# Performance work log

Measured on AMD Instinct MI355X. Metric: run time of the kernel, lower is better.

The kernel has to match this reference:

```python
import jax, jax.numpy as jnp
import numpy as np

N = 20000
E = 320000
IN_FEAT = 256
HID = 256
OUT_FEAT = 128


def setup_inputs() -> dict:
    key = jax.random.key(0)
    ks = jax.random.split(key, 10)
    inp = {
        "x": jax.random.normal(ks[0], (N, IN_FEAT), dtype=jnp.float32),
        "edge_src": jax.random.randint(ks[1], (E,), 0, N, dtype=jnp.int32),
        "edge_dst": jax.random.randint(ks[2], (E,), 0, N, dtype=jnp.int32),
        "edge_w": jax.random.uniform(ks[3], (E,), dtype=jnp.float32),
        # params (Linear weights stored as [out, in], torch convention)
        "W_emb": jax.random.normal(ks[4], (HID, IN_FEAT), dtype=jnp.float32) / np.sqrt(IN_FEAT),
        "W_gc1": jax.random.normal(ks[5], (HID, 2 * HID), dtype=jnp.float32) / np.sqrt(2 * HID),
        "b_gc1": jnp.zeros((HID,), dtype=jnp.float32),
        "W_gc2": jax.random.normal(ks[6], (HID, 2 * HID), dtype=jnp.float32) / np.sqrt(2 * HID),
        "b_gc2": jnp.zeros((HID,), dtype=jnp.float32),
        "W_fc": jax.random.normal(ks[7], (OUT_FEAT, HID), dtype=jnp.float32) / np.sqrt(HID),
    }
    return inp


def reference(x, edge_src, edge_dst, edge_w, W_emb, W_gc1, b_gc1, W_gc2, b_gc2, W_fc):
    n = x.shape[0]

    def adj_mul(h):
        msgs = h[edge_src] * edge_w[:, None]           # [E, hid]
        return jax.ops.segment_sum(msgs, edge_dst, num_segments=n)

    def gconv(h, W, b):
        cat = jnp.concatenate([h, adj_mul(h)], axis=1)  # [N, 2*hid]
        return cat @ W.T + b

    h = x @ W_emb.T                                    # embedding (no bias)
    h = h + jax.nn.relu(gconv(h, W_gc1, b_gc1))        # residual (dropout = eval identity)
    h = h + jax.nn.relu(gconv(h, W_gc2, b_gc2))
    out = h @ W_fc.T                                   # fc_last (no bias)
    out = out / jnp.sqrt(jnp.sum(out * out, axis=1, keepdims=True))
    return out
```

## Files before the change

### kernel.cpp

```cpp
#include <hip/hip_runtime.h>
#include <math.h>

#define N_NODES 20000
#define E_EDGES 320000
#define HID 256
#define OUT_FEAT 128
#define MPAD 20224
#define CAP 64

#define BK 64
#define LSTR 72

typedef __attribute__((ext_vector_type(8))) __bf16 bf16x8;
typedef __attribute__((ext_vector_type(4))) float floatx4;


#define EMB_BLK 632
#define SCAT_BLK 1250
#define CONV_BLK 144

__global__ __launch_bounds__(256) void front_kernel(
    const float* __restrict__ x,
    const float* __restrict__ wembf,
    __bf16* __restrict__ hb0,
    const int* __restrict__ src, const int* __restrict__ dst,
    const float* __restrict__ w, int* __restrict__ counts,
    int2* __restrict__ edges,
    const float* __restrict__ w1f, const float* __restrict__ w2f,
    const float* __restrict__ wfcf,
    __bf16* __restrict__ w1b, __bf16* __restrict__ w2b,
    __bf16* __restrict__ wfcb)
{
    __shared__ __bf16 As[64 * LSTR];
    __shared__ __bf16 Bs[128 * LSTR];
    const int bid = blockIdx.x;
    const int tid = threadIdx.x;

    if (bid < EMB_BLK) {
        const int row0 = (bid >> 1) * 64;
        const int col0 = (bid & 1) * 128;
        const int wv = tid >> 6, l = tid & 63, lr = l & 15, lq = l >> 4;
        const int wm = wv & 1, wn = wv >> 1;

        floatx4 acc[2][4];
#pragma unroll
        for (int i = 0; i < 2; i++)
#pragma unroll
            for (int j = 0; j < 4; j++) acc[i][j] = (floatx4){0.f, 0.f, 0.f, 0.f};

        const int srow = tid >> 3;
        const int skq = (tid & 7) * 8;

        for (int kc = 0; kc < 256; kc += BK) {
#pragma unroll
            for (int r = 0; r < 2; r++) {
                int row = r * 32 + srow;
                int grow = row0 + row;
                float4 v0 = make_float4(0.f, 0.f, 0.f, 0.f), v1 = v0;
                if (grow < N_NODES) {
                    const float* xp = x + (size_t)grow * HID + kc + skq;
                    v0 = *(const float4*)xp;
                    v1 = *(const float4*)(xp + 4);
                }
                bf16x8 o;
                o[0] = (__bf16)v0.x; o[1] = (__bf16)v0.y; o[2] = (__bf16)v0.z; o[3] = (__bf16)v0.w;
                o[4] = (__bf16)v1.x; o[5] = (__bf16)v1.y; o[6] = (__bf16)v1.z; o[7] = (__bf16)v1.w;
                *(bf16x8*)&As[row * LSTR + skq] = o;
            }
#pragma unroll
            for (int r = 0; r < 4; r++) {
                int row = r * 32 + srow;
                const float* wp = wembf + (size_t)(col0 + row) * 256 + kc + skq;
                float4 v0 = *(const float4*)wp;
                float4 v1 = *(const float4*)(wp + 4);
                bf16x8 o;
                o[0] = (__bf16)v0.x; o[1] = (__bf16)v0.y; o[2] = (__bf16)v0.z; o[3] = (__bf16)v0.w;
                o[4] = (__bf16)v1.x; o[5] = (__bf16)v1.y; o[6] = (__bf16)v1.z; o[7] = (__bf16)v1.w;
                *(bf16x8*)&Bs[row * LSTR + skq] = o;
            }
            __syncthreads();
#pragma unroll
            for (int s = 0; s < 2; s++) {
                bf16x8 af[2], bfr[4];
#pragma unroll
                for (int mt = 0; mt < 2; mt++)
                    af[mt] = *(const bf16x8*)&As[(wm * 32 + mt * 16 + lr) * LSTR + s * 32 + lq * 8];
#pragma unroll
                for (int nt = 0; nt < 4; nt++)
                    bfr[nt] = *(const bf16x8*)&Bs[(wn * 64 + nt * 16 + lr) * LSTR + s * 32 + lq * 8];
#pragma unroll
                for (int mt = 0; mt < 2; mt++)
#pragma unroll
                    for (int nt = 0; nt < 4; nt++)
                        acc[mt][nt] = __builtin_amdgcn_mfma_f32_16x16x32_bf16(af[mt], bfr[nt], acc[mt][nt], 0, 0, 0);
            }
            __syncthreads();
        }
#pragma unroll
        for (int nt = 0; nt < 4; nt++) {
            const int col = col0 + wn * 64 + nt * 16 + lr;
#pragma unroll
            for (int mt = 0; mt < 2; mt++) {
                const int row = row0 + wm * 32 + mt * 16 + lq * 4;
#pragma unroll
                for (int r = 0; r < 4; r++)
                    hb0[(size_t)(row + r) * HID + col] = (__bf16)acc[mt][nt][r];
            }
        }
    } else if (bid < EMB_BLK + SCAT_BLK) {
        int e = (bid - EMB_BLK) * 256 + tid;
        int d = dst[e];
        int p = atomicAdd(&counts[d], 1);
        edges[(size_t)d * CAP + p] = make_int2(src[e], __float_as_int(w[e]));
    } else {
        const size_t gi = ((size_t)(bid - EMB_BLK - SCAT_BLK) * 256 + tid) * 8;
        const size_t s1 = 131072, s2 = 262144;
        const float* srcp; __bf16* dstp; size_t off;
        if (gi < s1)      { srcp = w1f; dstp = w1b; off = gi; }
        else if (gi < s2) { srcp = w2f; dstp = w2b; off = gi - s1; }
        else              { srcp = wfcf; dstp = wfcb; off = gi - s2; }
        float4 v0 = *(const float4*)(srcp + off);
        float4 v1 = *(const float4*)(srcp + off + 4);
        bf16x8 o;
        o[0] = (__bf16)v0.x; o[1] = (__bf16)v0.y; o[2] = (__bf16)v0.z; o[3] = (__bf16)v0.w;
        o[4] = (__bf16)v1.x; o[5] = (__bf16)v1.y; o[6] = (__bf16)v1.z; o[7] = (__bf16)v1.w;
        *(bf16x8*)(dstp + off) = o;
    }
}


__global__ __launch_bounds__(256) void aggregate_kernel(
    const __bf16* __restrict__ h, const int* __restrict__ counts,
    const int2* __restrict__ edges, __bf16* __restrict__ agg) {
    const int w = threadIdx.x >> 6, lane = threadIdx.x & 63;
    const int half = lane >> 5, lh = lane & 31;
    const int d = blockIdx.x * 8 + w * 2 + half;
    const size_t base = (size_t)d * CAP;
    const int cnt = counts[d];
    const int iters = (cnt + 15) >> 4;
    float acc[8];
#pragma unroll
    for (int q = 0; q < 8; q++) acc[q] = 0.f;

    for (int it = 0; it < iters; ++it) {
        const int jb = it * 16;
        const int2* ep = edges + base + jb;
        int4 eh[8];
#pragma unroll
        for (int u = 0; u < 8; u++) eh[u] = *(const int4*)(ep + u * 2);
        int sidx[16]; float wv[16];
#pragma unroll
        for (int u = 0; u < 8; u++) {
            const bool m0 = (jb + u * 2)     < cnt;
            const bool m1 = (jb + u * 2 + 1) < cnt;
            sidx[u * 2]     = m0 ? eh[u].x : 0;
            wv[u * 2]       = m0 ? __int_as_float(eh[u].y) : 0.f;
            sidx[u * 2 + 1] = m1 ? eh[u].z : 0;
            wv[u * 2 + 1]   = m1 ? __int_as_float(eh[u].w) : 0.f;
        }
        bf16x8 hv[16];
#pragma unroll
        for (int u = 0; u < 16; u++)
            hv[u] = *(const bf16x8*)(h + (size_t)sidx[u] * HID + lh * 8);
#pragma unroll
        for (int u = 0; u < 16; u++) {
#pragma unroll
            for (int q = 0; q < 8; q++)
                acc[q] = fmaf(wv[u], (float)hv[u][q], acc[q]);
        }
    }
    bf16x8 o;
#pragma unroll
    for (int q = 0; q < 8; q++) o[q] = (__bf16)acc[q];
    *(bf16x8*)(agg + (size_t)d * HID + lh * 8) = o;
}


__global__ __launch_bounds__(256) void gconv1_kernel(
    const __bf16* __restrict__ hp,
    const __bf16* __restrict__ ag,
    const __bf16* __restrict__ W,
    const float* __restrict__ bias,
    __bf16* __restrict__ hn)
{
    __shared__ __bf16 As[64 * LSTR];
    __shared__ __bf16 Bs[128 * LSTR];
    const int tid = threadIdx.x;
    const int row0 = blockIdx.y * 64;
    const int col0 = blockIdx.x * 128;
    const int wv = tid >> 6, l = tid & 63, lr = l & 15, lq = l >> 4;
    const int wm = wv & 1, wn = wv >> 1;

    floatx4 acc[2][4];
#pragma unroll
    for (int i = 0; i < 2; i++)
#pragma unroll
        for (int j = 0; j < 4; j++) acc[i][j] = (floatx4){0.f, 0.f, 0.f, 0.f};

    const int srow = tid >> 3;
    const int skq = (tid & 7) * 8;

    for (int kc = 0; kc < 512; kc += BK) {
        const __bf16* Asrc = (kc >= 256) ? ag : hp;
        const int ks = kc & 255;
#pragma unroll
        for (int r = 0; r < 2; r++) {
            int row = r * 32 + srow;
            *(bf16x8*)&As[row * LSTR + skq] =
                *(const bf16x8*)(Asrc + (size_t)(row0 + row) * HID + ks + skq);
        }
#pragma unroll
        for (int r = 0; r < 4; r++) {
            int row = r * 32 + srow;
            *(bf16x8*)&Bs[row * LSTR + skq] =
                *(const bf16x8*)(W + (size_t)(col0 + row) * 512 + kc + skq);
        }
        __syncthreads();
#pragma unroll
        for (int s = 0; s < 2; s++) {
            bf16x8 af[2], bfr[4];
#pragma unroll
            for (int mt = 0; mt < 2; mt++)
                af[mt] = *(const bf16x8*)&As[(wm * 32 + mt * 16 + lr) * LSTR + s * 32 + lq * 8];
#pragma unroll
            for (int nt = 0; nt < 4; nt++)
                bfr[nt] = *(const bf16x8*)&Bs[(wn * 64 + nt * 16 + lr) * LSTR + s * 32 + lq * 8];
#pragma unroll
            for (int mt = 0; mt < 2; mt++)
#pragma unroll
                for (int nt = 0; nt < 4; nt++)
                    acc[mt][nt] = __builtin_amdgcn_mfma_f32_16x16x32_bf16(af[mt], bfr[nt], acc[mt][nt], 0, 0, 0);
        }
        __syncthreads();
    }

#pragma unroll
    for (int nt = 0; nt < 4; nt++) {
        const int col = col0 + wn * 64 + nt * 16 + lr;
        const float b = bias[col];
#pragma unroll
        for (int mt = 0; mt < 2; mt++) {
            const int row = row0 + wm * 32 + mt * 16 + lq * 4;
#pragma unroll
            for (int r = 0; r < 4; r++) {
                float res = (float)hp[(size_t)(row + r) * HID + col];
                float v = res + fmaxf(acc[mt][nt][r] + b, 0.f);
                hn[(size_t)(row + r) * HID + col] = (__bf16)v;
            }
        }
    }
}


#define TSTR 264

__global__ __launch_bounds__(512) void gconv_fc_kernel(
    const __bf16* __restrict__ hp,
    const __bf16* __restrict__ ag,
    const __bf16* __restrict__ W,
    const float* __restrict__ bias,
    const __bf16* __restrict__ Wfc,
    float* __restrict__ outp)
{
    __shared__ __bf16 smem[64 * LSTR + 256 * LSTR];
    __bf16* As = smem;
    __bf16* Bs = smem + 64 * LSTR;
    const int tid = threadIdx.x;
    const int row0 = blockIdx.x * 64;
    const int wv = tid >> 6, l = tid & 63, lr = l & 15, lq = l >> 4;
    const int wm = wv & 1, wn4 = wv >> 1;

    floatx4 acc[2][4];
#pragma unroll
    for (int i = 0; i < 2; i++)
#pragma unroll
        for (int j = 0; j < 4; j++) acc[i][j] = (floatx4){0.f, 0.f, 0.f, 0.f};

    const int srow = tid >> 3;
    const int skq = (tid & 7) * 8;

    for (int kc = 0; kc < 512; kc += BK) {
        const __bf16* Asrc = (kc >= 256) ? ag : hp;
        const int ks = kc & 255;
        *(bf16x8*)&As[srow * LSTR + skq] =
            *(const bf16x8*)(Asrc + (size_t)(row0 + srow) * HID + ks + skq);
#pragma unroll
        for (int r = 0; r < 4; r++) {
            int row = r * 64 + srow;
            *(bf16x8*)&Bs[row * LSTR + skq] =
                *(const bf16x8*)(W + (size_t)row * 512 + kc + skq);
        }
        __syncthreads();
#pragma unroll
        for (int s = 0; s < 2; s++) {
            bf16x8 af[2], bfr[4];
#pragma unroll
            for (int mt = 0; mt < 2; mt++)
                af[mt] = *(const bf16x8*)&As[(wm * 32 + mt * 16 + lr) * LSTR + s * 32 + lq * 8];
#pragma unroll
            for (int nt = 0; nt < 4; nt++)
                bfr[nt] = *(const bf16x8*)&Bs[(wn4 * 64 + nt * 16 + lr) * LSTR + s * 32 + lq * 8];
#pragma unroll
            for (int mt = 0; mt < 2; mt++)
#pragma unroll
                for (int nt = 0; nt < 4; nt++)
                    acc[mt][nt] = __builtin_amdgcn_mfma_f32_16x16x32_bf16(af[mt], bfr[nt], acc[mt][nt], 0, 0, 0);
        }
        __syncthreads();
    }

    __bf16 (*tile)[TSTR] = (__bf16(*)[TSTR])smem;
#pragma unroll
    for (int nt = 0; nt < 4; nt++) {
        const int col = wn4 * 64 + nt * 16 + lr;
        const float b = bias[col];
#pragma unroll
        for (int mt = 0; mt < 2; mt++) {
            const int lrow = wm * 32 + mt * 16 + lq * 4;
#pragma unroll
            for (int r = 0; r < 4; r++) {
                float res = (float)hp[(size_t)(row0 + lrow + r) * HID + col];
                float v = res + fmaxf(acc[mt][nt][r] + b, 0.f);
                tile[lrow + r][col] = (__bf16)v;
            }
        }
    }
    __syncthreads();

    if (wv < 4) {
        floatx4 facc[8];
#pragma unroll
        for (int j = 0; j < 8; j++) facc[j] = (floatx4){0.f, 0.f, 0.f, 0.f};
#pragma unroll
        for (int kt = 0; kt < 256; kt += 32) {
            bf16x8 a = *(const bf16x8*)&tile[wv * 16 + lr][kt + lq * 8];
            bf16x8 bf8[8];
#pragma unroll
            for (int nt = 0; nt < 8; nt++)
                bf8[nt] = *(const bf16x8*)(Wfc + (size_t)(nt * 16 + lr) * 256 + kt + lq * 8);
#pragma unroll
            for (int nt = 0; nt < 8; nt++)
                facc[nt] = __builtin_amdgcn_mfma_f32_16x16x32_bf16(a, bf8[nt], facc[nt], 0, 0, 0);
        }
        float s[4];
#pragma unroll
        for (int r = 0; r < 4; r++) {
            float t = 0.f;
#pragma unroll
            for (int nt = 0; nt < 8; nt++) t = fmaf(facc[nt][r], facc[nt][r], t);
            s[r] = t;
        }
#pragma unroll
        for (int mask = 1; mask <= 8; mask <<= 1) {
#pragma unroll
            for (int r = 0; r < 4; r++) s[r] += __shfl_xor(s[r], mask);
        }
        float inv[4];
#pragma unroll
        for (int r = 0; r < 4; r++) inv[r] = rsqrtf(s[r]);
#pragma unroll
        for (int r = 0; r < 4; r++) {
            int row = row0 + wv * 16 + lq * 4 + r;
            if (row >= N_NODES) continue;
#pragma unroll
            for (int nt = 0; nt < 8; nt++)
                outp[(size_t)row * OUT_FEAT + nt * 16 + lr] = facc[nt][r] * inv[r];
        }
    }
}


extern "C" void kernel_launch(void* const* d_in, const int* in_sizes, int n_in,
                              void* d_out, int out_size, void* d_ws, size_t ws_size,
                              hipStream_t stream) {
    const float* x        = (const float*)d_in[0];
    const int*   edge_src = (const int*)d_in[1];
    const int*   edge_dst = (const int*)d_in[2];
    const float* edge_w   = (const float*)d_in[3];
    const float* W_emb    = (const float*)d_in[4];
    const float* W_gc1    = (const float*)d_in[5];
    const float* b_gc1    = (const float*)d_in[6];
    const float* W_gc2    = (const float*)d_in[7];
    const float* b_gc2    = (const float*)d_in[8];
    const float* W_fc     = (const float*)d_in[9];
    float* out = (float*)d_out;

    char* p = (char*)d_ws;
    const size_t HROW = (size_t)MPAD * HID;
    __bf16* hb0   = (__bf16*)p;             p += HROW * 2;
    __bf16* hb1   = (__bf16*)p;             p += HROW * 2;
    __bf16* aggb  = (__bf16*)p;             p += HROW * 2;
    __bf16* w1b   = (__bf16*)p;             p += 131072 * 2;
    __bf16* w2b   = (__bf16*)p;             p += 131072 * 2;
    __bf16* wfcb  = (__bf16*)p;             p += 32768 * 2;
    int2*   edges = (int2*)p;               p += (size_t)N_NODES * CAP * 8;
    int*    counts = (int*)p;               p += (size_t)MPAD * 4;

    hipMemsetAsync(counts, 0, (size_t)MPAD * 4, stream);

    front_kernel<<<EMB_BLK + SCAT_BLK + CONV_BLK, 256, 0, stream>>>(
        x, W_emb, hb0, edge_src, edge_dst, edge_w, counts, edges,
        W_gc1, W_gc2, W_fc, w1b, w2b, wfcb);

    aggregate_kernel<<<N_NODES / 8, 256, 0, stream>>>(hb0, counts, edges, aggb);

    gconv1_kernel<<<dim3(2, MPAD / 64), 256, 0, stream>>>(hb0, aggb, w1b, b_gc1, hb1);

    aggregate_kernel<<<N_NODES / 8, 256, 0, stream>>>(hb1, counts, edges, aggb);

    gconv_fc_kernel<<<MPAD / 64, 512, 0, stream>>>(hb1, aggb, w2b, b_gc2, wfcb, out);
}
```

Baseline: 202.9 us.

## Gather int8 per-row quantized node features in aggregation instead of bf16

The embedding and first gconv kernels now produce full 256-column row tiles per block (512 threads, one block per 64 rows). Each also writes an int8 shadow copy of every node row with a per-row scale. The aggregation kernels gather these int8 rows and fold the scale into the edge weight, halving the bytes read per neighbour gather. The cost is extra quantization work and an extra shared-memory pass in the GEMM epilogues, plus lower precision in the aggregated messages.

```diff
diff --git a/kernel.cpp b/kernel.cpp
--- a/kernel.cpp
+++ b/kernel.cpp
@@ -10,19 +10,56 @@
 
 #define BK 64
 #define LSTR 72
+#define TSTR 264
 
 typedef __attribute__((ext_vector_type(8))) __bf16 bf16x8;
 typedef __attribute__((ext_vector_type(4))) float floatx4;
 
-
-#define EMB_BLK 632
-#define SCAT_BLK 1250
-#define CONV_BLK 144
-
-__global__ __launch_bounds__(256) void front_kernel(
+__device__ __forceinline__ void write_int8_shadow(
+    const __bf16 (*tile)[TSTR], int row0, int tid,
+    unsigned char* __restrict__ h8, float* __restrict__ scl) {
+    const int row = tid >> 3;
+    const int seg = tid & 7;
+    float vals[32];
+    float mx = 0.f;
+#pragma unroll
+    for (int j = 0; j < 32; j++) {
+        float v = (float)tile[row][seg * 32 + j];
+        vals[j] = v;
+        mx = fmaxf(mx, fabsf(v));
+    }
+#pragma unroll
+    for (int m = 1; m <= 4; m <<= 1) mx = fmaxf(mx, __shfl_xor(mx, m));
+    const float enc = mx > 0.f ? 127.f / mx : 0.f;
+    unsigned int pk[8];
+#pragma unroll
+    for (int g = 0; g < 8; g++) {
+        unsigned int wd = 0;
+#pragma unroll
+        for (int j = 0; j < 4; j++) {
+            int q = (int)rintf(vals[g * 4 + j] * enc);
+            q = q > 127 ? 127 : (q < -127 ? -127 : q);
+            wd |= ((unsigned int)(q & 0xff)) << (8 * j);
+        }
+        pk[g] = wd;
+    }
+    unsigned char* dstp = h8 + (size_t)(row0 + row) * HID + seg * 32;
+    *(int4*)dstp        = make_int4(pk[0], pk[1], pk[2], pk[3]);
+    *(int4*)(dstp + 16) = make_int4(pk[4], pk[5], pk[6], pk[7]);
+    if (seg == 0) scl[row0 + row] = mx * (1.f / 127.f);
+}
+
+
+#define EMB_BLK 316
+#define SCAT_BLK 625
+#define CONV_BLK 72
+
+__global__ __launch_bounds__(512) void front_kernel(
     const float* __restrict__ x,
     const float* __restrict__ wembf,
     __bf16* __restrict__ hb0,
+    unsigned char* __restrict__ h8,
+    float* __restrict__ scl,
     const int* __restrict__ src, const int* __restrict__ dst,
     const float* __restrict__ w, int* __restrict__ counts,
     int2* __restrict__ edges,
@@ -31,16 +68,16 @@
     __bf16* __restrict__ w1b, __bf16* __restrict__ w2b,
     __bf16* __restrict__ wfcb)
 {
-    __shared__ __bf16 As[64 * LSTR];
-    __shared__ __bf16 Bs[128 * LSTR];
+    __shared__ __bf16 smem[64 * LSTR + 256 * LSTR];
     const int bid = blockIdx.x;
     const int tid = threadIdx.x;
 
     if (bid < EMB_BLK) {
-        const int row0 = (bid >> 1) * 64;
-        const int col0 = (bid & 1) * 128;
+        __bf16* As = smem;
+        __bf16* Bs = smem + 64 * LSTR;
+        const int row0 = bid * 64;
         const int wv = tid >> 6, l = tid & 63, lr = l & 15, lq = l >> 4;
-        const int wm = wv & 1, wn = wv >> 1;
+        const int wm = wv & 1, wn4 = wv >> 1;
 
         floatx4 acc[2][4];
 #pragma unroll
@@ -52,10 +89,8 @@
         const int skq = (tid & 7) * 8;
 
         for (int kc = 0; kc < 256; kc += BK) {
-#pragma unroll
-            for (int r = 0; r < 2; r++) {
-                int row = r * 32 + srow;
-                int grow = row0 + row;
+            {
+                int grow = row0 + srow;
                 float4 v0 = make_float4(0.f, 0.f, 0.f, 0.f), v1 = v0;
                 if (grow < N_NODES) {
                     const float* xp = x + (size_t)grow * HID + kc + skq;
@@ -65,12 +100,12 @@
                 bf16x8 o;
                 o[0] = (__bf16)v0.x; o[1] = (__bf16)v0.y; o[2] = (__bf16)v0.z; o[3] = (__bf16)v0.w;
                 o[4] = (__bf16)v1.x; o[5] = (__bf16)v1.y; o[6] = (__bf16)v1.z; o[7] = (__bf16)v1.w;
-                *(bf16x8*)&As[row * LSTR + skq] = o;
+                *(bf16x8*)&As[srow * LSTR + skq] = o;
             }
 #pragma unroll
             for (int r = 0; r < 4; r++) {
-                int row = r * 32 + srow;
-                const float* wp = wembf + (size_t)(col0 + row) * 256 + kc + skq;
+                int row = r * 64 + srow;
+                const float* wp = wembf + (size_t)row * 256 + kc + skq;
                 float4 v0 = *(const float4*)wp;
                 float4 v1 = *(const float4*)(wp + 4);
                 bf16x8 o;
@@ -87,7 +122,7 @@
                     af[mt] = *(const bf16x8*)&As[(wm * 32 + mt * 16 + lr) * LSTR + s * 32 + lq * 8];
 #pragma unroll
                 for (int nt = 0; nt < 4; nt++)
-                    bfr[nt] = *(const bf16x8*)&Bs[(wn * 64 + nt * 16 + lr) * LSTR + s * 32 + lq * 8];
+                    bfr[nt] = *(const bf16x8*)&Bs[(wn4 * 64 + nt * 16 + lr) * LSTR + s * 32 + lq * 8];
 #pragma unroll
                 for (int mt = 0; mt < 2; mt++)
 #pragma unroll
@@ -96,24 +131,30 @@
             }
             __syncthreads();
         }
+        __bf16 (*tile)[TSTR] = (__bf16(*)[TSTR])smem;
 #pragma unroll
         for (int nt = 0; nt < 4; nt++) {
-            const int col = col0 + wn * 64 + nt * 16 + lr;
+            const int col = wn4 * 64 + nt * 16 + lr;
 #pragma unroll
             for (int mt = 0; mt < 2; mt++) {
-                const int row = row0 + wm * 32 + mt * 16 + lq * 4;
-#pragma unroll
-                for (int r = 0; r < 4; r++)
-                    hb0[(size_t)(row + r) * HID + col] = (__bf16)acc[mt][nt][r];
-            }
-        }
+                const int lrow = wm * 32 + mt * 16 + lq * 4;
+#pragma unroll
+                for (int r = 0; r < 4; r++) {
+                    float v = acc[mt][nt][r];
+                    hb0[(size_t)(row0 + lrow + r) * HID + col] = (__bf16)v;
+                    tile[lrow + r][col] = (__bf16)v;
+                }
+            }
+        }
+        __syncthreads();
+        write_int8_shadow(tile, row0, tid, h8, scl);
     } else if (bid < EMB_BLK + SCAT_BLK) {
-        int e = (bid - EMB_BLK) * 256 + tid;
+        int e = (bid - EMB_BLK) * 512 + tid;
         int d = dst[e];
         int p = atomicAdd(&counts[d], 1);
         edges[(size_t)d * CAP + p] = make_int2(src[e], __float_as_int(w[e]));
     } else {
-        const size_t gi = ((size_t)(bid - EMB_BLK - SCAT_BLK) * 256 + tid) * 8;
+        const size_t gi = ((size_t)(bid - EMB_BLK - SCAT_BLK) * 512 + tid) * 8;
         const size_t s1 = 131072, s2 = 262144;
         const float* srcp; __bf16* dstp; size_t off;
         if (gi < s1)      { srcp = w1f; dstp = w1b; off = gi; }
@@ -130,7 +171,8 @@
 
 
 __global__ __launch_bounds__(256) void aggregate_kernel(
-    const __bf16* __restrict__ h, const int* __restrict__ counts,
+    const unsigned char* __restrict__ h8, const float* __restrict__ scl,
+    const int* __restrict__ counts,
     const int2* __restrict__ edges, __bf16* __restrict__ agg) {
     const int w = threadIdx.x >> 6, lane = threadIdx.x & 63;
     const int half = lane >> 5, lh = lane & 31;
@@ -148,25 +190,35 @@
         int4 eh[8];
 #pragma unroll
         for (int u = 0; u < 8; u++) eh[u] = *(const int4*)(ep + u * 2);
-        int sidx[16]; float wv[16];
+        int sidx[16]; float ew[16];
 #pragma unroll
         for (int u = 0; u < 8; u++) {
             const bool m0 = (jb + u * 2)     < cnt;
             const bool m1 = (jb + u * 2 + 1) < cnt;
             sidx[u * 2]     = m0 ? eh[u].x : 0;
-            wv[u * 2]       = m0 ? __int_as_float(eh[u].y) : 0.f;
+            ew[u * 2]       = m0 ? __int_as_float(eh[u].y) : 0.f;
             sidx[u * 2 + 1] = m1 ? eh[u].z : 0;
-            wv[u * 2 + 1]   = m1 ? __int_as_float(eh[u].w) : 0.f;
-        }
-        bf16x8 hv[16];
+            ew[u * 2 + 1]   = m1 ? __int_as_float(eh[u].w) : 0.f;
+        }
+        float ws[16];
+#pragma unroll
+        for (int u = 0; u < 16; u++) ws[u] = ew[u] * scl[sidx[u]];
+        uint2 hv[16];
 #pragma unroll
         for (int u = 0; u < 16; u++)
-            hv[u] = *(const bf16x8*)(h + (size_t)sidx[u] * HID + lh * 8);
+            hv[u] = *(const uint2*)(h8 + (size_t)sidx[u] * HID + lh * 8);
 #pragma unroll
         for (int u = 0; u < 16; u++) {
-#pragma unroll
-            for (int q = 0; q < 8; q++)
-                acc[q] = fmaf(wv[u], (float)hv[u][q], acc[q]);
+            const unsigned int a = hv[u].x, b = hv[u].y;
+            const float wu = ws[u];
+            acc[0] = fmaf(wu, (float)(int)(signed char)(a),       acc[0]);
+            acc[1] = fmaf(wu, (float)(int)(signed char)(a >> 8),  acc[1]);
+            acc[2] = fmaf(wu, (float)(int)(signed char)(a >> 16), acc[2]);
+            acc[3] = fmaf(wu, (float)(int)(signed char)(a >> 24), acc[3]);
+            acc[4] = fmaf(wu, (float)(int)(signed char)(b),       acc[4]);
+            acc[5] = fmaf(wu, (float)(int)(signed char)(b >> 8),  acc[5]);
+            acc[6] = fmaf(wu, (float)(int)(signed char)(b >> 16), acc[6]);
+            acc[7] = fmaf(wu, (float)(int)(signed char)(b >> 24), acc[7]);
         }
     }
     bf16x8 o;
@@ -176,20 +228,22 @@
 }
 
 
-__global__ __launch_bounds__(256) void gconv1_kernel(
+__global__ __launch_bounds__(512) void gconv1_kernel(
     const __bf16* __restrict__ hp,
     const __bf16* __restrict__ ag,
     const __bf16* __restrict__ W,
     const float* __restrict__ bias,
-    __bf16* __restrict__ hn)
+    __bf16* __restrict__ hn,
+    unsigned char* __restrict__ h8,
+    float* __restrict__ scl)
 {
-    __shared__ __bf16 As[64 * LSTR];
-    __shared__ __bf16 Bs[128 * LSTR];
+    __shared__ __bf16 smem[64 * LSTR + 256 * LSTR];
+    __bf16* As = smem;
+    __bf16* Bs = smem + 64 * LSTR;
     const int tid = threadIdx.x;
-    const int row0 = blockIdx.y * 64;
-    const int col0 = blockIdx.x * 128;
+    const int row0 = blockIdx.x * 64;
     const int wv = tid >> 6, l = tid & 63, lr = l & 15, lq = l >> 4;
-    const int wm = wv & 1, wn = wv >> 1;
+    const int wm = wv & 1, wn4 = wv >> 1;
 
     floatx4 acc[2][4];
 #pragma unroll
@@ -203,17 +257,13 @@
     for (int kc = 0; kc < 512; kc += BK) {
         const __bf16* Asrc = (kc >= 256) ? ag : hp;
         const int ks = kc & 255;
-#pragma unroll
-        for (int r = 0; r < 2; r++) {
-            int row = r * 32 + srow;
-            *(bf16x8*)&As[row * LSTR + skq] =
-                *(const bf16x8*)(Asrc + (size_t)(row0 + row) * HID + ks + skq);
-        }
+        *(bf16x8*)&As[srow * LSTR + skq] =
+            *(const bf16x8*)(Asrc + (size_t)(row0 + srow) * HID + ks + skq);
 #pragma unroll
         for (int r = 0; r < 4; r++) {
-            int row = r * 32 + srow;
+            int row = r * 64 + srow;
             *(bf16x8*)&Bs[row * LSTR + skq] =
-                *(const bf16x8*)(W + (size_t)(col0 + row) * 512 + kc + skq);
+                *(const bf16x8*)(W + (size_t)row * 512 + kc + skq);
         }
         __syncthreads();
 #pragma unroll
@@ -224,7 +274,7 @@
                 af[mt] = *(const bf16x8*)&As[(wm * 32 + mt * 16 + lr) * LSTR + s * 32 + lq * 8];
 #pragma unroll
             for (int nt = 0; nt < 4; nt++)
-                bfr[nt] = *(const bf16x8*)&Bs[(wn * 64 + nt * 16 + lr) * LSTR + s * 32 + lq * 8];
+                bfr[nt] = *(const bf16x8*)&Bs[(wn4 * 64 + nt * 16 + lr) * LSTR + s * 32 + lq * 8];
 #pragma unroll
             for (int mt = 0; mt < 2; mt++)
 #pragma unroll
@@ -234,25 +284,27 @@
         __syncthreads();
     }
 
+    __bf16 (*tile)[TSTR] = (__bf16(*)[TSTR])smem;
 #pragma unroll
     for (int nt = 0; nt < 4; nt++) {
-        const int col = col0 + wn * 64 + nt * 16 + lr;
+        const int col = wn4 * 64 + nt * 16 + lr;
         const float b = bias[col];
 #pragma unroll
         for (int mt = 0; mt < 2; mt++) {
-            const int row = row0 + wm * 32 + mt * 16 + lq * 4;
+            const int lrow = wm * 32 + mt * 16 + lq * 4;
 #pragma unroll
             for (int r = 0; r < 4; r++) {
-                float res = (float)hp[(size_t)(row + r) * HID + col];
+                float res = (float)hp[(size_t)(row0 + lrow + r) * HID + col];
                 float v = res + fmaxf(acc[mt][nt][r] + b, 0.f);
-                hn[(size_t)(row + r) * HID + col] = (__bf16)v;
-            }
-        }
-    }
-}
-
-
-#define TSTR 264
+                hn[(size_t)(row0 + lrow + r) * HID + col] = (__bf16)v;
+                tile[lrow + r][col] = (__bf16)v;
+            }
+        }
+    }
+    __syncthreads();
+    write_int8_shadow(tile, row0, tid, h8, scl);
+}
+
 
 __global__ __launch_bounds__(512) void gconv_fc_kernel(
     const __bf16* __restrict__ hp,
@@ -390,6 +442,8 @@
     __bf16* hb0   = (__bf16*)p;             p += HROW * 2;
     __bf16* hb1   = (__bf16*)p;             p += HROW * 2;
     __bf16* aggb  = (__bf16*)p;             p += HROW * 2;
+    unsigned char* h8 = (unsigned char*)p;  p += HROW;
+    float*  scl   = (float*)p;              p += (size_t)MPAD * 4;
     __bf16* w1b   = (__bf16*)p;             p += 131072 * 2;
     __bf16* w2b   = (__bf16*)p;             p += 131072 * 2;
     __bf16* wfcb  = (__bf16*)p;             p += 32768 * 2;
@@ -398,15 +452,15 @@
 
     hipMemsetAsync(counts, 0, (size_t)MPAD * 4, stream);
 
-    front_kernel<<<EMB_BLK + SCAT_BLK + CONV_BLK, 256, 0, stream>>>(
-        x, W_emb, hb0, edge_src, edge_dst, edge_w, counts, edges,
+    front_kernel<<<EMB_BLK + SCAT_BLK + CONV_BLK, 512, 0, stream>>>(
+        x, W_emb, hb0, h8, scl, edge_src, edge_dst, edge_w, counts, edges,
         W_gc1, W_gc2, W_fc, w1b, w2b, wfcb);
 
-    aggregate_kernel<<<N_NODES / 8, 256, 0, stream>>>(hb0, counts, edges, aggb);
-
-    gconv1_kernel<<<dim3(2, MPAD / 64), 256, 0, stream>>>(hb0, aggb, w1b, b_gc1, hb1);
-
-    aggregate_kernel<<<N_NODES / 8, 256, 0, stream>>>(hb1, counts, edges, aggb);
+    aggregate_kernel<<<N_NODES / 8, 256, 0, stream>>>(h8, scl, counts, edges, aggb);
+
+    gconv1_kernel<<<MPAD / 64, 512, 0, stream>>>(hb0, aggb, w1b, b_gc1, hb1, h8, scl);
+
+    aggregate_kernel<<<N_NODES / 8, 256, 0, stream>>>(h8, scl, counts, edges, aggb);
 
     gconv_fc_kernel<<<MPAD / 64, 512, 0, stream>>>(hb1, aggb, w2b, b_gc2, wfcb, out);
 }
```

Result: no change. 202.8 us (median of 2 runs) (-0.0%).
